# Optimization experiments

Measured on AMD Instinct MI355X. Metric: run time of the kernel, lower is better.

The kernel has to match this reference:

```python
import jax, jax.numpy as jnp
import numpy as np
import math

EMBED_DIM = 1024
NUM_HEADS = 16
HEAD_DIM = EMBED_DIM // NUM_HEADS
SEGMENT_LENGTHS = [2048, 4096]
DILATION_RATES = [1, 2]
B, N = 1, 8192
IS_CAUSAL = True


def setup_inputs() -> dict:
    key = jax.random.key(0)
    ks = jax.random.split(key, 12)
    def w(k):
        return (jax.random.normal(k, (EMBED_DIM, EMBED_DIM), dtype=jnp.float32) * 0.02)
    inp = {
        'query': jax.random.normal(ks[0], (B, N, EMBED_DIM), dtype=jnp.float32),
        'key':   jax.random.normal(ks[1], (B, N, EMBED_DIM), dtype=jnp.float32),
        'value': jax.random.normal(ks[2], (B, N, EMBED_DIM), dtype=jnp.float32),
        'Wq': w(ks[3]), 'bq': jnp.zeros((EMBED_DIM,), jnp.float32),
        'Wk': w(ks[4]), 'bk': jnp.zeros((EMBED_DIM,), jnp.float32),
        'Wv': w(ks[5]), 'bv': jnp.zeros((EMBED_DIM,), jnp.float32),
        'Wo': w(ks[6]), 'bo': jnp.zeros((EMBED_DIM,), jnp.float32),
    }
    return inp


def _dilated_group_attention(q, k, v, seg_len, dilation, offset, causal):
    # q,k,v: [B, N, Hg, D] -> dilated block attention within segments
    b, n, hg, d = q.shape
    nseg = n // seg_len
    m = seg_len // dilation  # dilated subsequence length per segment
    idx = offset + dilation * jnp.arange(m)  # positions inside a segment
    def gather(x):
        return x.reshape(b, nseg, seg_len, hg, d)[:, :, idx]  # [B,nseg,m,Hg,D]
    qs, ks_, vs = gather(q), gather(k), gather(v)
    scale = 1.0 / math.sqrt(d)
    # [B,nseg,Hg,m,m]
    scores = jnp.einsum('bnihd,bnjhd->bnhij', qs, ks_) * scale
    if causal:
        mask = jnp.tril(jnp.ones((m, m), dtype=bool))
        scores = jnp.where(mask, scores, jnp.finfo(scores.dtype).min)
    attn = jax.nn.softmax(scores, axis=-1)
    out = jnp.einsum('bnhij,bnjhd->bnihd', attn, vs)  # [B,nseg,m,Hg,D]
    # scatter dilated outputs back to full segment positions (others zero)
    full = jnp.zeros((b, nseg, seg_len, hg, d), dtype=out.dtype)
    full = full.at[:, :, idx].set(out)
    return full.reshape(b, n, hg, d)


def reference(query, key, value, Wq, bq, Wk, bk, Wv, bv, Wo, bo):
    b, n, e = query.shape
    q = query @ Wq.T + bq
    k = key @ Wk.T + bk
    v = value @ Wv.T + bv
    q = q.reshape(b, n, NUM_HEADS, HEAD_DIM)
    k = k.reshape(b, n, NUM_HEADS, HEAD_DIM)
    v = v.reshape(b, n, NUM_HEADS, HEAD_DIM)
    num_groups = len(SEGMENT_LENGTHS)
    hpg = NUM_HEADS // num_groups  # heads per (segment, dilation) group
    outs = []
    for g in range(num_groups):
        s, r = SEGMENT_LENGTHS[g], DILATION_RATES[g]
        off = g % r
        hsl = slice(g * hpg, (g + 1) * hpg)
        outs.append(_dilated_group_attention(q[:, :, hsl], k[:, :, hsl], v[:, :, hsl],
                                             s, r, off, IS_CAUSAL))
    attn_out = jnp.concatenate(outs, axis=2).reshape(b, n, e)
    return attn_out @ Wo.T + bo
```

## Files before the change

### kernel.cpp

```cpp
#include <hip/hip_runtime.h>
#include <hip/hip_bf16.h>

typedef __attribute__((ext_vector_type(8))) __bf16 bf16x8;
typedef __attribute__((ext_vector_type(8))) unsigned short us8;
typedef __attribute__((ext_vector_type(4))) float f32x4;
typedef __attribute__((ext_vector_type(16))) float f32x16;
typedef __attribute__((ext_vector_type(2))) unsigned int uint2v;

#define N_TOK 8192
#define EMB 1024

static __device__ __forceinline__ unsigned short f2bf(float f) {
  union { __bf16 b; unsigned short u; } c;
  c.b = (__bf16)f;
  return c.u;
}

static __device__ __forceinline__ f32x4 mfma16(bf16x8 a, bf16x8 b, f32x4 c) {
  return __builtin_amdgcn_mfma_f32_16x16x32_bf16(a, b, c, 0, 0, 0);
}
static __device__ __forceinline__ f32x16 mfma32(bf16x8 a, bf16x8 b, f32x16 c) {
  return __builtin_amdgcn_mfma_f32_32x32x16_bf16(a, b, c, 0, 0, 0);
}
static __device__ __forceinline__ unsigned int cvtpk(float lo, float hi) {
  unsigned int r;
  asm("v_cvt_pk_bf16_f32 %0, %1, %2" : "=v"(r) : "v"(lo), "v"(hi));
  return r;
}
static __device__ __forceinline__ void gload16(const unsigned short* g, unsigned short* l) {
  __builtin_amdgcn_global_load_lds(
      (const __attribute__((address_space(1))) unsigned int*)g,
      (__attribute__((address_space(3))) unsigned int*)l, 16, 0, 0);
}

__global__ __launch_bounds__(256) void convall(
    const float* __restrict__ X0, const float* __restrict__ X1, const float* __restrict__ X2,
    const float* __restrict__ W0, const float* __restrict__ W1,
    const float* __restrict__ W2, const float* __restrict__ W3,
    unsigned short* __restrict__ Dq, unsigned short* __restrict__ Dk,
    unsigned short* __restrict__ Dv, unsigned short* __restrict__ Wb)
{
  const int bid = blockIdx.x;
  const float* src;
  unsigned short* dst;
  long base;
  if (bid < 6144) {
    const int t = bid >> 11;
    const int b = bid & 2047;
    src = (t == 0) ? X0 : (t == 1) ? X1 : X2;
    dst = (t == 0) ? Dq : (t == 1) ? Dk : Dv;
    base = ((long)b * 256 + threadIdx.x) * 16;
  } else {
    const int r = bid - 6144;
    const int t = r >> 8;
    const int b = r & 255;
    src = (t == 0) ? W0 : (t == 1) ? W1 : (t == 2) ? W2 : W3;
    dst = Wb + (size_t)t * EMB * EMB;
    base = ((long)b * 256 + threadIdx.x) * 16;
  }
  float4 f0 = *(const float4*)(src + base);
  float4 f1 = *(const float4*)(src + base + 4);
  float4 f2 = *(const float4*)(src + base + 8);
  float4 f3 = *(const float4*)(src + base + 12);
  us8 p0, p1;
  p0[0]=f2bf(f0.x); p0[1]=f2bf(f0.y); p0[2]=f2bf(f0.z); p0[3]=f2bf(f0.w);
  p0[4]=f2bf(f1.x); p0[5]=f2bf(f1.y); p0[6]=f2bf(f1.z); p0[7]=f2bf(f1.w);
  p1[0]=f2bf(f2.x); p1[1]=f2bf(f2.y); p1[2]=f2bf(f2.z); p1[3]=f2bf(f2.w);
  p1[4]=f2bf(f3.x); p1[5]=f2bf(f3.y); p1[6]=f2bf(f3.z); p1[7]=f2bf(f3.w);
  *(us8*)(dst + base)     = p0;
  *(us8*)(dst + base + 8) = p1;
}

__global__ __launch_bounds__(256) void qkv_gemm7(
    const unsigned short* __restrict__ Xq, const unsigned short* __restrict__ Xk,
    const unsigned short* __restrict__ Xv, const unsigned short* __restrict__ Wb,
    const float* __restrict__ bq, const float* __restrict__ bk, const float* __restrict__ bv,
    unsigned short* __restrict__ O0, unsigned short* __restrict__ O1, unsigned short* __restrict__ O2)
{
  __shared__ __align__(16) unsigned short As[128 * 32];
  __shared__ __align__(16) unsigned short Bs[128 * 32];

  const int z = blockIdx.z;
  const unsigned short* X = (z == 0) ? Xq : (z == 1) ? Xk : Xv;
  const unsigned short* W = Wb + (size_t)z * EMB * EMB;
  const float* bias = (z == 0) ? bq : (z == 1) ? bk : bv;

  const int lin  = blockIdx.x;
  const int work = (lin & 7) * 64 + (lin >> 3);
  const long brow = (long)(work >> 3) * 128;
  const long bcol = (long)(work & 7) * 128;

  const int tid  = threadIdx.x;
  const int lane = tid & 63;
  const int w    = tid >> 6;
  const int wrb  = (w >> 1) * 64;
  const int wcb  = (w & 1) * 64;
  const int r16  = lane & 15;
  const int kq   = (lane >> 4) * 8;
  const int rq   = (lane >> 4) * 4;

  const int srow = lane >> 2;
  const int scol = (lane & 3) * 8;
  const unsigned short* Ag0 = X + (brow + w*32      + srow) * (long)EMB + scol;
  const unsigned short* Ag1 = X + (brow + w*32 + 16 + srow) * (long)EMB + scol;
  const unsigned short* Bg0 = W + (bcol + w*32      + srow) * (long)EMB + scol;
  const unsigned short* Bg1 = W + (bcol + w*32 + 16 + srow) * (long)EMB + scol;
  unsigned short* Al0 = As + w * 1024;
  unsigned short* Al1 = As + w * 1024 + 512;
  unsigned short* Bl0 = Bs + w * 1024;
  unsigned short* Bl1 = Bs + w * 1024 + 512;

  const f32x4 zz = {0.f, 0.f, 0.f, 0.f};
  f32x4 acc[4][4];
#pragma unroll
  for (int i = 0; i < 4; ++i)
#pragma unroll
    for (int j = 0; j < 4; ++j) acc[i][j] = zz;

  for (int k0 = 0; k0 < EMB; k0 += 32) {
    __syncthreads();
    gload16(Ag0 + k0, Al0);
    gload16(Ag1 + k0, Al1);
    gload16(Bg0 + k0, Bl0);
    gload16(Bg1 + k0, Bl1);
    __syncthreads();

    bf16x8 av[4], bv_[4];
#pragma unroll
    for (int mi = 0; mi < 4; ++mi) av[mi]  = *(const bf16x8*)&As[(wrb + mi*16 + r16)*32 + kq];
#pragma unroll
    for (int ni = 0; ni < 4; ++ni) bv_[ni] = *(const bf16x8*)&Bs[(wcb + ni*16 + r16)*32 + kq];
    if (z == 2) {
#pragma unroll
      for (int mi = 0; mi < 4; ++mi)
#pragma unroll
        for (int ni = 0; ni < 4; ++ni)
          acc[mi][ni] = mfma16(bv_[ni], av[mi], acc[mi][ni]);
    } else {
#pragma unroll
      for (int mi = 0; mi < 4; ++mi)
#pragma unroll
        for (int ni = 0; ni < 4; ++ni)
          acc[mi][ni] = mfma16(av[mi], bv_[ni], acc[mi][ni]);
    }
  }

  if (z == 2) {
#pragma unroll
    for (int ni = 0; ni < 4; ++ni)
#pragma unroll
      for (int jr = 0; jr < 4; ++jr) {
        const long c = bcol + wcb + ni*16 + rq + jr;
        const float bval = bias[c];
#pragma unroll
        for (int mi = 0; mi < 4; ++mi) {
          long rt = brow + wrb + mi*16 + r16;
          if (c >= 512) {
            const long seg = rt >> 12;
            const long pp = rt & 4095;
            rt = (seg << 12) + ((pp & 1) ? (pp >> 1) : 2048 + (pp >> 1));
          }
          O2[c * (long)N_TOK + rt] = f2bf(acc[mi][ni][jr] + bval);
        }
      }
  } else {
    unsigned short* O = (z == 0) ? O0 : O1;
#pragma unroll
    for (int ni = 0; ni < 4; ++ni) {
      const long col = bcol + wcb + ni*16 + r16;
      const float bval = bias[col];
#pragma unroll
      for (int mi = 0; mi < 4; ++mi)
#pragma unroll
        for (int jr = 0; jr < 4; ++jr) {
          const long row = brow + wrb + mi*16 + rq + jr;
          O[row * (long)EMB + col] = f2bf(acc[mi][ni][jr] + bval);
        }
    }
  }
}

__global__ __launch_bounds__(128) void attn_dilated7(
    const unsigned short* __restrict__ Qp, const unsigned short* __restrict__ Kp,
    const unsigned short* __restrict__ Vt, unsigned short* __restrict__ AO)
{
  __shared__ __align__(16) unsigned short Ks[2][64][72];
  __shared__ __align__(16) unsigned short Vs[2][64][72];

  const int z   = blockIdx.z;
  const int g1  = (z >= 4);
  const int dil = g1 ? 2 : 1;
  const int off = g1 ? 1 : 0;
  const long segb = g1 ? (long)(z - 4) * 4096 : (long)z * 2048;
  const int h   = (g1 ? 8 : 0) + blockIdx.y;
  const int h64 = h * 64;

  const int bx   = (int)blockIdx.x;
  const int tid  = threadIdx.x;
  const int lane = tid & 63;
  const int w    = tid >> 6;
  const int q5   = lane & 31;
  const int hh   = lane >> 5;

  const int srow = tid >> 1;
  const int sc   = (tid & 1) * 32;

  const float SC2 = 0.18033688011112042f;

#pragma unroll
  for (int ph = 0; ph < 2; ++ph) {
    const int hf = ph ? bx : 31 - bx;
    const int qq = hf*64 + w*32 + q5;
    const long qrow = segb + off + (long)dil * qq;

    bf16x8 qf[4];
    {
      const unsigned short* qsrc = Qp + qrow * EMB + h64 + 8*hh;
#pragma unroll
      for (int s = 0; s < 4; ++s) qf[s] = *(const bf16x8*)(qsrc + 16*s);
    }

    float l_run = 0.f;
    f32x16 o0, o1;
#pragma unroll
    for (int r = 0; r < 16; ++r) { o0[r] = 0.f; o1[r] = 0.f; }

    us8 kr0, kr1, kr2, kr3, vr0, vr1, vr2, vr3;
    {
      const long gk = segb + off + (long)dil * srow;
      const unsigned short* ksrc = Kp + gk*EMB + h64 + sc;
      kr0 = *(const us8*)ksrc;        kr1 = *(const us8*)(ksrc + 8);
      kr2 = *(const us8*)(ksrc + 16); kr3 = *(const us8*)(ksrc + 24);
      const unsigned short* vsrc = Vt + (long)(h64 + srow)*N_TOK + segb + sc;
      vr0 = *(const us8*)vsrc;        vr1 = *(const us8*)(vsrc + 8);
      vr2 = *(const us8*)(vsrc + 16); vr3 = *(const us8*)(vsrc + 24);
      *(us8*)&Ks[0][srow][sc]    = kr0; *(us8*)&Ks[0][srow][sc+8]  = kr1;
      *(us8*)&Ks[0][srow][sc+16] = kr2; *(us8*)&Ks[0][srow][sc+24] = kr3;
      *(us8*)&Vs[0][srow][sc]    = vr0; *(us8*)&Vs[0][srow][sc+8]  = vr1;
      *(us8*)&Vs[0][srow][sc+16] = vr2; *(us8*)&Vs[0][srow][sc+24] = vr3;
    }
    __syncthreads();
    int cur = 0;

    for (int j = 0; j <= hf; ++j) {
      if (j < hf) {
        const long gk = segb + off + (long)dil * ((j+1)*64 + srow);
        const unsigned short* ksrc = Kp + gk*EMB + h64 + sc;
        kr0 = *(const us8*)ksrc;        kr1 = *(const us8*)(ksrc + 8);
        kr2 = *(const us8*)(ksrc + 16); kr3 = *(const us8*)(ksrc + 24);
        const unsigned short* vsrc = Vt + (long)(h64 + srow)*N_TOK + segb + (j+1)*64 + sc;
        vr0 = *(const us8*)vsrc;        vr1 = *(const us8*)(vsrc + 8);
        vr2 = *(const us8*)(vsrc + 16); vr3 = *(const us8*)(vsrc + 24);
      }

      f32x16 sa0, sa1;
#pragma unroll
      for (int r = 0; r < 16; ++r) { sa0[r] = 0.f; sa1[r] = 0.f; }
      __builtin_amdgcn_s_setprio(1);
#pragma unroll
      for (int s = 0; s < 4; ++s) {
        bf16x8 ka = *(const bf16x8*)&Ks[cur][q5][16*s + 8*hh];
        sa0 = mfma32(ka, qf[s], sa0);
      }
#pragma unroll
      for (int s = 0; s < 4; ++s) {
        bf16x8 kb = *(const bf16x8*)&Ks[cur][32 + q5][16*s + 8*hh];
        sa1 = mfma32(kb, qf[s], sa1);
      }
      __builtin_amdgcn_s_setprio(0);

      const bool diag   = (j == hf);
      const bool do_kb1 = (j < hf) || (w == 1);

      float sv[32];
#pragma unroll
      for (int r = 0; r < 16; ++r) {
        const int kof = (r&3) + 8*(r>>2);
        float v = fmaf(sa0[r], SC2, -8.0f);
        if (diag && (j*64 + kof + 4*hh > qq)) v = -1e30f;
        sv[r] = v;
      }
      if (do_kb1) {
#pragma unroll
        for (int r = 0; r < 16; ++r) {
          const int kof = (r&3) + 8*(r>>2);
          float v = fmaf(sa1[r], SC2, -8.0f);
          if (diag && (j*64 + 32 + kof + 4*hh > qq)) v = -1e30f;
          sv[16+r] = v;
        }
      }

      float psum = 0.f;
#pragma unroll
      for (int i = 0; i < 16; ++i) { float e = exp2f(sv[i]); sv[i] = e; psum += e; }
      if (do_kb1) {
#pragma unroll
        for (int i = 16; i < 32; ++i) { float e = exp2f(sv[i]); sv[i] = e; psum += e; }
      }
      {
        union { float f; unsigned int u; } pc; pc.f = psum;
        uint2v ps = __builtin_amdgcn_permlane32_swap(pc.u, pc.u, false, false);
        union { unsigned int u; float f; } a0, a1;
        a0.u = ps[0]; a1.u = ps[1];
        psum = a0.f + a1.f;
      }
      l_run += psum;

#pragma unroll
      for (int ks = 0; ks < 4; ++ks) {
        if (ks >= 2 && !do_kb1) continue;
        const unsigned int pk0 = cvtpk(sv[8*ks+0], sv[8*ks+1]);
        const unsigned int pk1 = cvtpk(sv[8*ks+2], sv[8*ks+3]);
        const unsigned int pk2 = cvtpk(sv[8*ks+4], sv[8*ks+5]);
        const unsigned int pk3 = cvtpk(sv[8*ks+6], sv[8*ks+7]);
        uint2v s02 = __builtin_amdgcn_permlane32_swap(pk0, pk2, false, false);
        uint2v s13 = __builtin_amdgcn_permlane32_swap(pk1, pk3, false, false);
        union { unsigned int wd[4]; bf16x8 v; } pu;
        pu.wd[0] = s02[0];
        pu.wd[1] = s13[0];
        pu.wd[2] = s02[1];
        pu.wd[3] = s13[1];
        __builtin_amdgcn_s_setprio(1);
        bf16x8 va = *(const bf16x8*)&Vs[cur][q5][16*ks + 8*hh];
        o0 = mfma32(va, pu.v, o0);
        bf16x8 vb = *(const bf16x8*)&Vs[cur][32 + q5][16*ks + 8*hh];
        o1 = mfma32(vb, pu.v, o1);
        __builtin_amdgcn_s_setprio(0);
      }

      if (j < hf) {
        *(us8*)&Ks[cur^1][srow][sc]    = kr0; *(us8*)&Ks[cur^1][srow][sc+8]  = kr1;
        *(us8*)&Ks[cur^1][srow][sc+16] = kr2; *(us8*)&Ks[cur^1][srow][sc+24] = kr3;
        *(us8*)&Vs[cur^1][srow][sc]    = vr0; *(us8*)&Vs[cur^1][srow][sc+8]  = vr1;
        *(us8*)&Vs[cur^1][srow][sc+16] = vr2; *(us8*)&Vs[cur^1][srow][sc+24] = vr3;
      }
      __syncthreads();
      cur ^= 1;
    }

    {
      const float inv = 1.f / l_run;
      unsigned short* dst = AO + qrow * EMB + h64;
#pragma unroll
      for (int r = 0; r < 16; ++r) {
        const int d = (r&3) + 8*(r>>2) + 4*hh;
        dst[d]      = f2bf(o0[r] * inv);
        dst[32 + d] = f2bf(o1[r] * inv);
      }
    }
  }
}

__global__ __launch_bounds__(256) void gemm_out4(
    const unsigned short* __restrict__ A, const unsigned short* __restrict__ Wb,
    const float* __restrict__ bias, float* __restrict__ outp)
{
  __shared__ __align__(16) unsigned short As[128 * 32];
  __shared__ __align__(16) unsigned short Bs[128 * 32];

  const int lin  = blockIdx.x;
  const int work = (lin & 7) * 64 + (lin >> 3);
  const long brow = (long)(work >> 3) * 128;
  const long bcol = (long)(work & 7) * 128;

  const int tid  = threadIdx.x;
  const int lane = tid & 63;
  const int w    = tid >> 6;
  const int wrb  = (w >> 1) * 64;
  const int wcb  = (w & 1) * 64;
  const int r16  = lane & 15;
  const int kq   = (lane >> 4) * 8;
  const int rq   = (lane >> 4) * 4;

  const int srow = lane >> 2;
  const int scol = (lane & 3) * 8;
  const unsigned short* Ag0 = A  + (brow + w*32      + srow) * (long)EMB + scol;
  const unsigned short* Ag1 = A  + (brow + w*32 + 16 + srow) * (long)EMB + scol;
  const unsigned short* Bg0 = Wb + (bcol + w*32      + srow) * (long)EMB + scol;
  const unsigned short* Bg1 = Wb + (bcol + w*32 + 16 + srow) * (long)EMB + scol;
  unsigned short* Al0 = As + w * 1024;
  unsigned short* Al1 = As + w * 1024 + 512;
  unsigned short* Bl0 = Bs + w * 1024;
  unsigned short* Bl1 = Bs + w * 1024 + 512;

  const f32x4 zz = {0.f, 0.f, 0.f, 0.f};
  f32x4 acc[4][4];
#pragma unroll
  for (int i = 0; i < 4; ++i)
#pragma unroll
    for (int j = 0; j < 4; ++j) acc[i][j] = zz;

  for (int k0 = 0; k0 < EMB; k0 += 32) {
    __syncthreads();
    gload16(Ag0 + k0, Al0);
    gload16(Ag1 + k0, Al1);
    gload16(Bg0 + k0, Bl0);
    gload16(Bg1 + k0, Bl1);
    __syncthreads();

    bf16x8 av[4], bv_[4];
#pragma unroll
    for (int mi = 0; mi < 4; ++mi) av[mi]  = *(const bf16x8*)&As[(wrb + mi*16 + r16)*32 + kq];
#pragma unroll
    for (int ni = 0; ni < 4; ++ni) bv_[ni] = *(const bf16x8*)&Bs[(wcb + ni*16 + r16)*32 + kq];
#pragma unroll
    for (int mi = 0; mi < 4; ++mi)
#pragma unroll
      for (int ni = 0; ni < 4; ++ni)
        acc[mi][ni] = mfma16(av[mi], bv_[ni], acc[mi][ni]);
  }

#pragma unroll
  for (int ni = 0; ni < 4; ++ni) {
    const long col = bcol + wcb + ni*16 + r16;
    const float bval = bias[col];
#pragma unroll
    for (int mi = 0; mi < 4; ++mi)
#pragma unroll
      for (int jr = 0; jr < 4; ++jr) {
        const long row = brow + wrb + mi*16 + rq + jr;
        outp[row * (long)EMB + col] = acc[mi][ni][jr] + bval;
      }
  }
}

extern "C" void kernel_launch(void* const* d_in, const int* in_sizes, int n_in,
                              void* d_out, int out_size, void* d_ws, size_t ws_size,
                              hipStream_t stream) {
  const float* query = (const float*)d_in[0];
  const float* key_  = (const float*)d_in[1];
  const float* value = (const float*)d_in[2];
  const float* Wq = (const float*)d_in[3];
  const float* bq = (const float*)d_in[4];
  const float* Wk = (const float*)d_in[5];
  const float* bk = (const float*)d_in[6];
  const float* Wv = (const float*)d_in[7];
  const float* bv = (const float*)d_in[8];
  const float* Wo = (const float*)d_in[9];
  const float* bo = (const float*)d_in[10];

  unsigned short* Qp  = (unsigned short*)d_ws;
  unsigned short* Kp  = Qp + (size_t)N_TOK * EMB;
  unsigned short* Vt  = Kp + (size_t)N_TOK * EMB;
  unsigned short* Wb  = Vt + (size_t)N_TOK * EMB;
  unsigned short* S   = Wb + (size_t)4 * EMB * EMB;
  unsigned short* Xbq = (unsigned short*)d_out;
  unsigned short* Xbk = Xbq + (size_t)N_TOK * EMB;
  unsigned short* Xbv = S;
  unsigned short* AO  = S;
  unsigned short* Wob = Wb + (size_t)3 * EMB * EMB;

  dim3 blk(256);

  hipLaunchKernelGGL(convall, dim3(7168), blk, 0, stream,
                     query, key_, value, Wq, Wk, Wv, Wo, Xbq, Xbk, Xbv, Wb);

  hipLaunchKernelGGL(qkv_gemm7, dim3(512, 1, 3), blk, 0, stream,
                     Xbq, Xbk, Xbv, Wb, bq, bk, bv, Qp, Kp, Vt);

  hipMemsetAsync(AO, 0, (size_t)N_TOK * EMB * 2, stream);

  hipLaunchKernelGGL(attn_dilated7, dim3(16, 8, 6), dim3(128), 0, stream, Qp, Kp, Vt, AO);

  hipLaunchKernelGGL(gemm_out4, dim3(512), blk, 0, stream, AO, Wob, bo, (float*)d_out);
}
```

Measured before the change: 220.3 us.

## Process both query tiles in one pass sharing K/V loads

The attention kernel used to run two sequential phases per block, each streaming K/V tiles from global into shared memory for its own query tile (long and short). Now both query tiles are handled in a single loop over K/V. The short tile reuses the K/V tiles already staged for the long tile, which removes the second round of global loads and barriers. This doubles the live accumulator and Q-fragment registers, which may raise register pressure, reduce occupancy or cause spills.

```diff
diff --git a/kernel.cpp b/kernel.cpp
--- a/kernel.cpp
+++ b/kernel.cpp
@@ -180,7 +180,7 @@
   }
 }
 
-__global__ __launch_bounds__(128) void attn_dilated7(
+__global__ __launch_bounds__(128) void attn_dilated8(
     const unsigned short* __restrict__ Qp, const unsigned short* __restrict__ Kp,
     const unsigned short* __restrict__ Vt, unsigned short* __restrict__ AO)
 {
@@ -202,94 +202,101 @@
   const int q5   = lane & 31;
   const int hh   = lane >> 5;
 
+  const int hfL = 31 - bx;
+  const int hfS = bx;
+
+  const int qqL = hfL*64 + w*32 + q5;
+  const int qqS = hfS*64 + w*32 + q5;
+  const long qrowL = segb + off + (long)dil * qqL;
+  const long qrowS = segb + off + (long)dil * qqS;
+
+  bf16x8 qfL[4], qfS[4];
+  {
+    const unsigned short* qsrc = Qp + qrowL * EMB + h64 + 8*hh;
+#pragma unroll
+    for (int s = 0; s < 4; ++s) qfL[s] = *(const bf16x8*)(qsrc + 16*s);
+    qsrc = Qp + qrowS * EMB + h64 + 8*hh;
+#pragma unroll
+    for (int s = 0; s < 4; ++s) qfS[s] = *(const bf16x8*)(qsrc + 16*s);
+  }
+
+  float lL = 0.f, lS = 0.f;
+  f32x16 oL0, oL1, oS0, oS1;
+#pragma unroll
+  for (int r = 0; r < 16; ++r) { oL0[r]=0.f; oL1[r]=0.f; oS0[r]=0.f; oS1[r]=0.f; }
+
   const int srow = tid >> 1;
   const int sc   = (tid & 1) * 32;
 
   const float SC2 = 0.18033688011112042f;
 
-#pragma unroll
-  for (int ph = 0; ph < 2; ++ph) {
-    const int hf = ph ? bx : 31 - bx;
-    const int qq = hf*64 + w*32 + q5;
-    const long qrow = segb + off + (long)dil * qq;
-
-    bf16x8 qf[4];
-    {
-      const unsigned short* qsrc = Qp + qrow * EMB + h64 + 8*hh;
-#pragma unroll
-      for (int s = 0; s < 4; ++s) qf[s] = *(const bf16x8*)(qsrc + 16*s);
-    }
-
-    float l_run = 0.f;
-    f32x16 o0, o1;
-#pragma unroll
-    for (int r = 0; r < 16; ++r) { o0[r] = 0.f; o1[r] = 0.f; }
-
-    us8 kr0, kr1, kr2, kr3, vr0, vr1, vr2, vr3;
-    {
-      const long gk = segb + off + (long)dil * srow;
+  us8 kr0, kr1, kr2, kr3, vr0, vr1, vr2, vr3;
+  {
+    const long gk = segb + off + (long)dil * srow;
+    const unsigned short* ksrc = Kp + gk*EMB + h64 + sc;
+    kr0 = *(const us8*)ksrc;        kr1 = *(const us8*)(ksrc + 8);
+    kr2 = *(const us8*)(ksrc + 16); kr3 = *(const us8*)(ksrc + 24);
+    const unsigned short* vsrc = Vt + (long)(h64 + srow)*N_TOK + segb + sc;
+    vr0 = *(const us8*)vsrc;        vr1 = *(const us8*)(vsrc + 8);
+    vr2 = *(const us8*)(vsrc + 16); vr3 = *(const us8*)(vsrc + 24);
+    *(us8*)&Ks[0][srow][sc]    = kr0; *(us8*)&Ks[0][srow][sc+8]  = kr1;
+    *(us8*)&Ks[0][srow][sc+16] = kr2; *(us8*)&Ks[0][srow][sc+24] = kr3;
+    *(us8*)&Vs[0][srow][sc]    = vr0; *(us8*)&Vs[0][srow][sc+8]  = vr1;
+    *(us8*)&Vs[0][srow][sc+16] = vr2; *(us8*)&Vs[0][srow][sc+24] = vr3;
+  }
+  __syncthreads();
+  int cur = 0;
+
+  for (int j = 0; j <= hfL; ++j) {
+    if (j < hfL) {
+      const long gk = segb + off + (long)dil * ((j+1)*64 + srow);
       const unsigned short* ksrc = Kp + gk*EMB + h64 + sc;
       kr0 = *(const us8*)ksrc;        kr1 = *(const us8*)(ksrc + 8);
       kr2 = *(const us8*)(ksrc + 16); kr3 = *(const us8*)(ksrc + 24);
-      const unsigned short* vsrc = Vt + (long)(h64 + srow)*N_TOK + segb + sc;
+      const unsigned short* vsrc = Vt + (long)(h64 + srow)*N_TOK + segb + (j+1)*64 + sc;
       vr0 = *(const us8*)vsrc;        vr1 = *(const us8*)(vsrc + 8);
       vr2 = *(const us8*)(vsrc + 16); vr3 = *(const us8*)(vsrc + 24);
-      *(us8*)&Ks[0][srow][sc]    = kr0; *(us8*)&Ks[0][srow][sc+8]  = kr1;
-      *(us8*)&Ks[0][srow][sc+16] = kr2; *(us8*)&Ks[0][srow][sc+24] = kr3;
-      *(us8*)&Vs[0][srow][sc]    = vr0; *(us8*)&Vs[0][srow][sc+8]  = vr1;
-      *(us8*)&Vs[0][srow][sc+16] = vr2; *(us8*)&Vs[0][srow][sc+24] = vr3;
-    }
-    __syncthreads();
-    int cur = 0;
-
-    for (int j = 0; j <= hf; ++j) {
-      if (j < hf) {
-        const long gk = segb + off + (long)dil * ((j+1)*64 + srow);
-        const unsigned short* ksrc = Kp + gk*EMB + h64 + sc;
-        kr0 = *(const us8*)ksrc;        kr1 = *(const us8*)(ksrc + 8);
-        kr2 = *(const us8*)(ksrc + 16); kr3 = *(const us8*)(ksrc + 24);
-        const unsigned short* vsrc = Vt + (long)(h64 + srow)*N_TOK + segb + (j+1)*64 + sc;
-        vr0 = *(const us8*)vsrc;        vr1 = *(const us8*)(vsrc + 8);
-        vr2 = *(const us8*)(vsrc + 16); vr3 = *(const us8*)(vsrc + 24);
-      }
-
-      f32x16 sa0, sa1;
-#pragma unroll
-      for (int r = 0; r < 16; ++r) { sa0[r] = 0.f; sa1[r] = 0.f; }
-      __builtin_amdgcn_s_setprio(1);
-#pragma unroll
-      for (int s = 0; s < 4; ++s) {
-        bf16x8 ka = *(const bf16x8*)&Ks[cur][q5][16*s + 8*hh];
-        sa0 = mfma32(ka, qf[s], sa0);
-      }
-#pragma unroll
-      for (int s = 0; s < 4; ++s) {
-        bf16x8 kb = *(const bf16x8*)&Ks[cur][32 + q5][16*s + 8*hh];
-        sa1 = mfma32(kb, qf[s], sa1);
-      }
-      __builtin_amdgcn_s_setprio(0);
-
-      const bool diag   = (j == hf);
-      const bool do_kb1 = (j < hf) || (w == 1);
-
+    }
+
+    const bool doS = (j <= hfS);
+
+    f32x16 saL0, saL1, saS0, saS1;
+#pragma unroll
+    for (int r = 0; r < 16; ++r) { saL0[r]=0.f; saL1[r]=0.f; saS0[r]=0.f; saS1[r]=0.f; }
+    __builtin_amdgcn_s_setprio(1);
+#pragma unroll
+    for (int s = 0; s < 4; ++s) {
+      bf16x8 ka = *(const bf16x8*)&Ks[cur][q5][16*s + 8*hh];
+      bf16x8 kb = *(const bf16x8*)&Ks[cur][32 + q5][16*s + 8*hh];
+      saL0 = mfma32(ka, qfL[s], saL0);
+      saL1 = mfma32(kb, qfL[s], saL1);
+      if (doS) {
+        saS0 = mfma32(ka, qfS[s], saS0);
+        saS1 = mfma32(kb, qfS[s], saS1);
+      }
+    }
+    __builtin_amdgcn_s_setprio(0);
+
+    {
+      const bool diag   = (j == hfL);
+      const bool do_kb1 = (j < hfL) || (w == 1);
       float sv[32];
 #pragma unroll
       for (int r = 0; r < 16; ++r) {
         const int kof = (r&3) + 8*(r>>2);
-        float v = fmaf(sa0[r], SC2, -8.0f);
-        if (diag && (j*64 + kof + 4*hh > qq)) v = -1e30f;
+        float v = fmaf(saL0[r], SC2, -8.0f);
+        if (diag && (j*64 + kof + 4*hh > qqL)) v = -1e30f;
         sv[r] = v;
       }
       if (do_kb1) {
 #pragma unroll
         for (int r = 0; r < 16; ++r) {
           const int kof = (r&3) + 8*(r>>2);
-          float v = fmaf(sa1[r], SC2, -8.0f);
-          if (diag && (j*64 + 32 + kof + 4*hh > qq)) v = -1e30f;
+          float v = fmaf(saL1[r], SC2, -8.0f);
+          if (diag && (j*64 + 32 + kof + 4*hh > qqL)) v = -1e30f;
           sv[16+r] = v;
         }
       }
-
       float psum = 0.f;
 #pragma unroll
       for (int i = 0; i < 16; ++i) { float e = exp2f(sv[i]); sv[i] = e; psum += e; }
@@ -304,8 +311,7 @@
         a0.u = ps[0]; a1.u = ps[1];
         psum = a0.f + a1.f;
       }
-      l_run += psum;
-
+      lL += psum;
 #pragma unroll
       for (int ks = 0; ks < 4; ++ks) {
         if (ks >= 2 && !do_kb1) continue;
@@ -316,37 +322,97 @@
         uint2v s02 = __builtin_amdgcn_permlane32_swap(pk0, pk2, false, false);
         uint2v s13 = __builtin_amdgcn_permlane32_swap(pk1, pk3, false, false);
         union { unsigned int wd[4]; bf16x8 v; } pu;
-        pu.wd[0] = s02[0];
-        pu.wd[1] = s13[0];
-        pu.wd[2] = s02[1];
-        pu.wd[3] = s13[1];
+        pu.wd[0] = s02[0]; pu.wd[1] = s13[0]; pu.wd[2] = s02[1]; pu.wd[3] = s13[1];
         __builtin_amdgcn_s_setprio(1);
         bf16x8 va = *(const bf16x8*)&Vs[cur][q5][16*ks + 8*hh];
-        o0 = mfma32(va, pu.v, o0);
+        oL0 = mfma32(va, pu.v, oL0);
         bf16x8 vb = *(const bf16x8*)&Vs[cur][32 + q5][16*ks + 8*hh];
-        o1 = mfma32(vb, pu.v, o1);
+        oL1 = mfma32(vb, pu.v, oL1);
         __builtin_amdgcn_s_setprio(0);
       }
-
-      if (j < hf) {
-        *(us8*)&Ks[cur^1][srow][sc]    = kr0; *(us8*)&Ks[cur^1][srow][sc+8]  = kr1;
-        *(us8*)&Ks[cur^1][srow][sc+16] = kr2; *(us8*)&Ks[cur^1][srow][sc+24] = kr3;
-        *(us8*)&Vs[cur^1][srow][sc]    = vr0; *(us8*)&Vs[cur^1][srow][sc+8]  = vr1;
-        *(us8*)&Vs[cur^1][srow][sc+16] = vr2; *(us8*)&Vs[cur^1][srow][sc+24] = vr3;
-      }
-      __syncthreads();
-      cur ^= 1;
-    }
-
-    {
-      const float inv = 1.f / l_run;
-      unsigned short* dst = AO + qrow * EMB + h64;
+    }
+
+    if (doS) {
+      const bool diag   = (j == hfS);
+      const bool do_kb1 = (j < hfS) || (w == 1);
+      float sv[32];
 #pragma unroll
       for (int r = 0; r < 16; ++r) {
-        const int d = (r&3) + 8*(r>>2) + 4*hh;
-        dst[d]      = f2bf(o0[r] * inv);
-        dst[32 + d] = f2bf(o1[r] * inv);
-      }
+        const int kof = (r&3) + 8*(r>>2);
+        float v = fmaf(saS0[r], SC2, -8.0f);
+        if (diag && (j*64 + kof + 4*hh > qqS)) v = -1e30f;
+        sv[r] = v;
+      }
+      if (do_kb1) {
+#pragma unroll
+        for (int r = 0; r < 16; ++r) {
+          const int kof = (r&3) + 8*(r>>2);
+          float v = fmaf(saS1[r], SC2, -8.0f);
+          if (diag && (j*64 + 32 + kof + 4*hh > qqS)) v = -1e30f;
+          sv[16+r] = v;
+        }
+      }
+      float psum = 0.f;
+#pragma unroll
+      for (int i = 0; i < 16; ++i) { float e = exp2f(sv[i]); sv[i] = e; psum += e; }
+      if (do_kb1) {
+#pragma unroll
+        for (int i = 16; i < 32; ++i) { float e = exp2f(sv[i]); sv[i] = e; psum += e; }
+      }
+      {
+        union { float f; unsigned int u; } pc; pc.f = psum;
+        uint2v ps = __builtin_amdgcn_permlane32_swap(pc.u, pc.u, false, false);
+        union { unsigned int u; float f; } a0, a1;
+        a0.u = ps[0]; a1.u = ps[1];
+        psum = a0.f + a1.f;
+      }
+      lS += psum;
+#pragma unroll
+      for (int ks = 0; ks < 4; ++ks) {
+        if (ks >= 2 && !do_kb1) continue;
+        const unsigned int pk0 = cvtpk(sv[8*ks+0], sv[8*ks+1]);
+        const unsigned int pk1 = cvtpk(sv[8*ks+2], sv[8*ks+3]);
+        const unsigned int pk2 = cvtpk(sv[8*ks+4], sv[8*ks+5]);
+        const unsigned int pk3 = cvtpk(sv[8*ks+6], sv[8*ks+7]);
+        uint2v s02 = __builtin_amdgcn_permlane32_swap(pk0, pk2, false, false);
+        uint2v s13 = __builtin_amdgcn_permlane32_swap(pk1, pk3, false, false);
+        union { unsigned int wd[4]; bf16x8 v; } pu;
+        pu.wd[0] = s02[0]; pu.wd[1] = s13[0]; pu.wd[2] = s02[1]; pu.wd[3] = s13[1];
+        __builtin_amdgcn_s_setprio(1);
+        bf16x8 va = *(const bf16x8*)&Vs[cur][q5][16*ks + 8*hh];
+        oS0 = mfma32(va, pu.v, oS0);
+        bf16x8 vb = *(const bf16x8*)&Vs[cur][32 + q5][16*ks + 8*hh];
+        oS1 = mfma32(vb, pu.v, oS1);
+        __builtin_amdgcn_s_setprio(0);
+      }
+    }
+
+    if (j < hfL) {
+      *(us8*)&Ks[cur^1][srow][sc]    = kr0; *(us8*)&Ks[cur^1][srow][sc+8]  = kr1;
+      *(us8*)&Ks[cur^1][srow][sc+16] = kr2; *(us8*)&Ks[cur^1][srow][sc+24] = kr3;
+      *(us8*)&Vs[cur^1][srow][sc]    = vr0; *(us8*)&Vs[cur^1][srow][sc+8]  = vr1;
+      *(us8*)&Vs[cur^1][srow][sc+16] = vr2; *(us8*)&Vs[cur^1][srow][sc+24] = vr3;
+    }
+    __syncthreads();
+    cur ^= 1;
+  }
+
+  {
+    const float invL = 1.f / lL;
+    unsigned short* dst = AO + qrowL * EMB + h64;
+#pragma unroll
+    for (int r = 0; r < 16; ++r) {
+      const int d = (r&3) + 8*(r>>2) + 4*hh;
+      dst[d]      = f2bf(oL0[r] * invL);
+      dst[32 + d] = f2bf(oL1[r] * invL);
+    }
+    const float invS = 1.f / lS;
+    dst = AO + qrowS * EMB + h64;
+#pragma unroll
+    for (int r = 0; r < 16; ++r) {
+      const int d = (r&3) + 8*(r>>2) + 4*hh;
+      dst[d]      = f2bf(oS0[r] * invS);
+      dst[32 + d] = f2bf(oS1[r] * invS);
     }
   }
 }
@@ -460,7 +526,7 @@
 
   hipMemsetAsync(AO, 0, (size_t)N_TOK * EMB * 2, stream);
 
-  hipLaunchKernelGGL(attn_dilated7, dim3(16, 8, 6), dim3(128), 0, stream, Qp, Kp, Vt, AO);
+  hipLaunchKernelGGL(attn_dilated8, dim3(16, 8, 6), dim3(128), 0, stream, Qp, Kp, Vt, AO);
 
   hipLaunchKernelGGL(gemm_out4, dim3(512), blk, 0, stream, AO, Wob, bo, (float*)d_out);
 }
```

After: 260.8 us. 1.18x slower.
